# Optimization experiments

Hardware: AMD Instinct MI355X
Metric: run time of the kernel (lower is better)

The kernel has to match this reference:

```python
import jax, jax.numpy as jnp
import numpy as np

BN_EPS = 1e-5


def setup_inputs() -> dict:
    key = jax.random.key(0)
    ks = jax.random.split(key, 6)
    N_IN, N_OUT, K3, P, C_IN, C_OUT = 100000, 200000, 27, 80000, 64, 64
    features = jax.random.normal(ks[0], (N_IN, C_IN), dtype=jnp.float32)
    weight = jax.random.normal(ks[1], (K3, C_IN, C_OUT), dtype=jnp.float32) * 0.05
    bias = jnp.zeros((C_OUT,), dtype=jnp.float32)
    gamma = jnp.ones((C_OUT,), dtype=jnp.float32)
    beta = jnp.zeros((C_OUT,), dtype=jnp.float32)
    pairs_in = jax.random.randint(ks[2], (K3, P), 0, N_IN, dtype=jnp.int32)
    pairs_out = jax.random.randint(ks[3], (K3, P), 0, N_OUT, dtype=jnp.int32)
    return {
        "features": features, "weight": weight, "bias": bias,
        "gamma": gamma, "beta": beta,
        "pairs_in": pairs_in, "pairs_out": pairs_out, "n_out": N_OUT,
    }


def reference(features, weight, bias, gamma, beta, pairs_in, pairs_out, n_out):
    # --- SparseInverseConv3d: gather -> per-offset GEMM -> scatter-add ---
    C_out = weight.shape[2]
    gathered = features[pairs_in]                      # [K3, P, C_in]
    prod = jnp.einsum('kpc,kcd->kpd', gathered, weight)  # [K3, P, C_out]
    out = jnp.zeros((n_out, C_out), dtype=features.dtype)
    out = out.at[pairs_out.reshape(-1)].add(prod.reshape(-1, C_out))
    out = out + bias                                   # [N_out, C_out]
    # --- BatchNorm1d (training mode: batch stats, biased var) ---
    mean = jnp.mean(out, axis=0)
    var = jnp.var(out, axis=0)
    y = (out - mean) * jax.lax.rsqrt(var + BN_EPS) * gamma + beta
    # --- ReLU ---
    return jnp.maximum(y, 0.0)
```

## Files before the change

kernel.cpp:

```cpp
#include <hip/hip_runtime.h>
#include <hip/hip_fp16.h>


#define C_DIM 64
#define LDS_STRIDE 72
#define ROW_STRIDE 68

typedef __bf16 bf16_t;
typedef bf16_t bf16x4 __attribute__((ext_vector_type(4)));
typedef bf16_t bf16x8 __attribute__((ext_vector_type(8)));
typedef float floatx4 __attribute__((ext_vector_type(4)));

__global__ __launch_bounds__(256)
void k_fprep(const float* __restrict__ f, bf16_t* __restrict__ fb, int total4)
{
    int i = blockIdx.x * 256 + threadIdx.x;
    if (i < total4) {
        float4 v = ((const float4*)f)[i];
        bf16x4 o;
        o[0] = (bf16_t)v.x; o[1] = (bf16_t)v.y;
        o[2] = (bf16_t)v.z; o[3] = (bf16_t)v.w;
        ((bf16x4*)fb)[i] = o;
    }
}

__global__ __launch_bounds__(256)
void k1_fp16(const float* __restrict__ features,
             const bf16_t* __restrict__ fbf16,
             const float* __restrict__ weight,
             const int* __restrict__ pairs_in,
             const int* __restrict__ pairs_out,
             __half* __restrict__ acc,
             int P, int rows_per_block, int use_bf16)
{
    __shared__ bf16_t Wt[C_DIM * LDS_STRIDE];
    __shared__ float  scratch[4][16 * ROW_STRIDE];

    const int k   = blockIdx.y;
    const int tid = threadIdx.x;

    const float* Wk = weight + (size_t)k * C_DIM * C_DIM;
    for (int i = tid; i < C_DIM * C_DIM; i += 256) {
        int c = i >> 6, d = i & 63;
        Wt[d * LDS_STRIDE + c] = (bf16_t)Wk[i];
    }
    __syncthreads();

    const int wave = tid >> 6;
    const int lane = tid & 63;
    const int quad = lane >> 4;
    const int col  = lane & 15;
    const int sub  = lane >> 5;
    const int c2   = lane & 31;
    float* ls = &scratch[wave][0];

    bf16x8 bfrag[2][4];
    #pragma unroll
    for (int ks = 0; ks < 2; ++ks)
        #pragma unroll
        for (int nt = 0; nt < 4; ++nt)
            bfrag[ks][nt] =
                *(const bf16x8*)&Wt[(col + 16 * nt) * LDS_STRIDE + quad * 8 + 32 * ks];

    const int* __restrict__ pin  = pairs_in  + (size_t)k * P;
    const int* __restrict__ pout = pairs_out + (size_t)k * P;

    const int p0   = blockIdx.x * rows_per_block;
    const int pend = min(p0 + rows_per_block, P);

    for (int base = p0 + wave * 16; base < pend; base += 64) {
        int prow    = base + col;
        int clamped = (prow < pend) ? prow : (pend - 1);
        int in_idx  = pin[clamped];
        int out_idx = pout[clamped];

        bf16x8 a0, a1;
        if (use_bf16) {
            const bf16_t* src = fbf16 + (size_t)in_idx * C_DIM + quad * 8;
            a0 = *(const bf16x8*)(src);
            a1 = *(const bf16x8*)(src + 32);
        } else {
            const float* src = features + (size_t)in_idx * C_DIM + quad * 8;
            float4 f0 = *(const float4*)(src);
            float4 f1 = *(const float4*)(src + 4);
            float4 f2 = *(const float4*)(src + 32);
            float4 f3 = *(const float4*)(src + 36);
            a0[0] = (bf16_t)f0.x; a0[1] = (bf16_t)f0.y; a0[2] = (bf16_t)f0.z; a0[3] = (bf16_t)f0.w;
            a0[4] = (bf16_t)f1.x; a0[5] = (bf16_t)f1.y; a0[6] = (bf16_t)f1.z; a0[7] = (bf16_t)f1.w;
            a1[0] = (bf16_t)f2.x; a1[1] = (bf16_t)f2.y; a1[2] = (bf16_t)f2.z; a1[3] = (bf16_t)f2.w;
            a1[4] = (bf16_t)f3.x; a1[5] = (bf16_t)f3.y; a1[6] = (bf16_t)f3.z; a1[7] = (bf16_t)f3.w;
        }

        floatx4 acc0 = {0.f, 0.f, 0.f, 0.f};
        floatx4 acc1 = {0.f, 0.f, 0.f, 0.f};
        floatx4 acc2 = {0.f, 0.f, 0.f, 0.f};
        floatx4 acc3 = {0.f, 0.f, 0.f, 0.f};

        acc0 = __builtin_amdgcn_mfma_f32_16x16x32_bf16(a0, bfrag[0][0], acc0, 0, 0, 0);
        acc0 = __builtin_amdgcn_mfma_f32_16x16x32_bf16(a1, bfrag[1][0], acc0, 0, 0, 0);
        acc1 = __builtin_amdgcn_mfma_f32_16x16x32_bf16(a0, bfrag[0][1], acc1, 0, 0, 0);
        acc1 = __builtin_amdgcn_mfma_f32_16x16x32_bf16(a1, bfrag[1][1], acc1, 0, 0, 0);
        acc2 = __builtin_amdgcn_mfma_f32_16x16x32_bf16(a0, bfrag[0][2], acc2, 0, 0, 0);
        acc2 = __builtin_amdgcn_mfma_f32_16x16x32_bf16(a1, bfrag[1][2], acc2, 0, 0, 0);
        acc3 = __builtin_amdgcn_mfma_f32_16x16x32_bf16(a0, bfrag[0][3], acc3, 0, 0, 0);
        acc3 = __builtin_amdgcn_mfma_f32_16x16x32_bf16(a1, bfrag[1][3], acc3, 0, 0, 0);

        #pragma unroll
        for (int r = 0; r < 4; ++r) {
            int m = quad * 4 + r;
            ls[m * ROW_STRIDE + col +  0] = acc0[r];
            ls[m * ROW_STRIDE + col + 16] = acc1[r];
            ls[m * ROW_STRIDE + col + 32] = acc2[r];
            ls[m * ROW_STRIDE + col + 48] = acc3[r];
        }
        asm volatile("s_waitcnt lgkmcnt(0)" ::: "memory");

        #pragma unroll
        for (int m2 = 0; m2 < 8; ++m2) {
            int m = m2 * 2 + sub;
            float2 v = *(const float2*)&ls[m * ROW_STRIDE + 2 * c2];
            __half2 h = __floats2half2_rn(v.x, v.y);
            int g = __shfl(out_idx, m);
            if (base + m < pend)
                unsafeAtomicAdd((__half2*)(acc + (size_t)g * C_DIM + 2 * c2), h);
        }
    }
}

__global__ __launch_bounds__(256)
void k2_stats_h(const __half* __restrict__ acc, float* __restrict__ sums,
                int n_rows)
{
    const int tid = threadIdx.x;
    const int c2  = tid & 31;
    const int sub = tid >> 5;

    float s0 = 0.f, s1 = 0.f, q0 = 0.f, q1 = 0.f;
    for (int r = blockIdx.x * 8 + sub; r < n_rows; r += gridDim.x * 8) {
        __half2 v = *(const __half2*)&acc[(size_t)r * C_DIM + 2 * c2];
        float x = __half2float(v.x), y = __half2float(v.y);
        s0 += x; q0 += x * x;
        s1 += y; q1 += y * y;
    }

    __shared__ float red[128];
    if (tid < 128) red[tid] = 0.f;
    __syncthreads();
    atomicAdd(&red[2 * c2], s0);
    atomicAdd(&red[2 * c2 + 1], s1);
    atomicAdd(&red[64 + 2 * c2], q0);
    atomicAdd(&red[64 + 2 * c2 + 1], q1);
    __syncthreads();
    if (tid < 128) atomicAdd(&sums[tid], red[tid]);
}

__global__ __launch_bounds__(256)
void k3_bn_relu_h(const __half* __restrict__ acc, float* __restrict__ out,
                  const float* __restrict__ sums,
                  const float* __restrict__ gamma, const float* __restrict__ beta,
                  int n_rows)
{
    int tid = blockIdx.x * 256 + threadIdx.x;
    int c2  = tid & 31;
    float inv_n = 1.0f / (float)n_rows;

    float sc[2], sh[2];
    #pragma unroll
    for (int j = 0; j < 2; ++j) {
        int ch    = 2 * c2 + j;
        float m   = sums[ch] * inv_n;
        float var = sums[64 + ch] * inv_n - m * m;
        float inv = rsqrtf(var + 1e-5f);
        float g   = gamma[ch] * inv;
        sc[j] = g;
        sh[j] = beta[ch] - m * g;
    }

    size_t total = (size_t)n_rows * (C_DIM / 2);
    for (size_t i = tid; i < total; i += (size_t)gridDim.x * 256) {
        __half2 v = ((const __half2*)acc)[i];
        float2 o;
        o.x = fmaxf(__half2float(v.x) * sc[0] + sh[0], 0.f);
        o.y = fmaxf(__half2float(v.y) * sc[1] + sh[1], 0.f);
        ((float2*)out)[i] = o;
    }
}

__global__ __launch_bounds__(256)
void k1_scatter_gemm(const float* __restrict__ features,
                     const float* __restrict__ weight,
                     const int* __restrict__ pairs_in,
                     const int* __restrict__ pairs_out,
                     float* __restrict__ out,
                     int P, int rows_per_block)
{
    __shared__ bf16_t Wt[C_DIM * LDS_STRIDE];
    const int k   = blockIdx.y;
    const int tid = threadIdx.x;
    const float* Wk = weight + (size_t)k * C_DIM * C_DIM;
    for (int i = tid; i < C_DIM * C_DIM; i += 256) {
        int c = i >> 6, d = i & 63;
        Wt[d * LDS_STRIDE + c] = (bf16_t)Wk[i];
    }
    __syncthreads();
    const int wave = tid >> 6, lane = tid & 63, quad = lane >> 4, col = lane & 15;
    bf16x8 bfrag[2][4];
    #pragma unroll
    for (int ks = 0; ks < 2; ++ks)
        #pragma unroll
        for (int nt = 0; nt < 4; ++nt)
            bfrag[ks][nt] =
                *(const bf16x8*)&Wt[(col + 16 * nt) * LDS_STRIDE + quad * 8 + 32 * ks];
    const int* __restrict__ pin  = pairs_in  + (size_t)k * P;
    const int* __restrict__ pout = pairs_out + (size_t)k * P;
    const int p0   = blockIdx.x * rows_per_block;
    const int pend = min(p0 + rows_per_block, P);
    for (int base = p0 + wave * 16; base < pend; base += 64) {
        int prow    = base + col;
        int clamped = (prow < pend) ? prow : (pend - 1);
        int in_idx  = pin[clamped];
        int out_idx = pout[clamped];
        const float* src = features + (size_t)in_idx * C_DIM + quad * 8;
        float4 f0 = *(const float4*)(src);
        float4 f1 = *(const float4*)(src + 4);
        float4 f2 = *(const float4*)(src + 32);
        float4 f3 = *(const float4*)(src + 36);
        bf16x8 a0, a1;
        a0[0] = (bf16_t)f0.x; a0[1] = (bf16_t)f0.y; a0[2] = (bf16_t)f0.z; a0[3] = (bf16_t)f0.w;
        a0[4] = (bf16_t)f1.x; a0[5] = (bf16_t)f1.y; a0[6] = (bf16_t)f1.z; a0[7] = (bf16_t)f1.w;
        a1[0] = (bf16_t)f2.x; a1[1] = (bf16_t)f2.y; a1[2] = (bf16_t)f2.z; a1[3] = (bf16_t)f2.w;
        a1[4] = (bf16_t)f3.x; a1[5] = (bf16_t)f3.y; a1[6] = (bf16_t)f3.z; a1[7] = (bf16_t)f3.w;
        floatx4 acc0 = {0.f,0.f,0.f,0.f}, acc1 = {0.f,0.f,0.f,0.f};
        floatx4 acc2 = {0.f,0.f,0.f,0.f}, acc3 = {0.f,0.f,0.f,0.f};
        acc0 = __builtin_amdgcn_mfma_f32_16x16x32_bf16(a0, bfrag[0][0], acc0, 0, 0, 0);
        acc0 = __builtin_amdgcn_mfma_f32_16x16x32_bf16(a1, bfrag[1][0], acc0, 0, 0, 0);
        acc1 = __builtin_amdgcn_mfma_f32_16x16x32_bf16(a0, bfrag[0][1], acc1, 0, 0, 0);
        acc1 = __builtin_amdgcn_mfma_f32_16x16x32_bf16(a1, bfrag[1][1], acc1, 0, 0, 0);
        acc2 = __builtin_amdgcn_mfma_f32_16x16x32_bf16(a0, bfrag[0][2], acc2, 0, 0, 0);
        acc2 = __builtin_amdgcn_mfma_f32_16x16x32_bf16(a1, bfrag[1][2], acc2, 0, 0, 0);
        acc3 = __builtin_amdgcn_mfma_f32_16x16x32_bf16(a0, bfrag[0][3], acc3, 0, 0, 0);
        acc3 = __builtin_amdgcn_mfma_f32_16x16x32_bf16(a1, bfrag[1][3], acc3, 0, 0, 0);
        #pragma unroll
        for (int r = 0; r < 4; ++r) {
            int m = quad * 4 + r;
            int g = __shfl(out_idx, m);
            if (base + m < pend) {
                float* dst = out + (size_t)g * C_DIM + col;
                unsafeAtomicAdd(dst +  0, acc0[r]);
                unsafeAtomicAdd(dst + 16, acc1[r]);
                unsafeAtomicAdd(dst + 32, acc2[r]);
                unsafeAtomicAdd(dst + 48, acc3[r]);
            }
        }
    }
}

__global__ __launch_bounds__(256)
void k2_stats(const float* __restrict__ acc, float* __restrict__ sums, int n_rows)
{
    int tid = threadIdx.x;
    int ch  = tid & 63;
    int sub = tid >> 6;
    float s = 0.f, s2 = 0.f;
    for (int r = blockIdx.x * 4 + sub; r < n_rows; r += gridDim.x * 4) {
        float v = acc[(size_t)r * C_DIM + ch];
        s  += v;
        s2 += v * v;
    }
    __shared__ float red[256];
    red[tid] = s;
    __syncthreads();
    if (tid < 64) {
        float t = red[tid] + red[tid + 64] + red[tid + 128] + red[tid + 192];
        atomicAdd(&sums[ch], t);
    }
    __syncthreads();
    red[tid] = s2;
    __syncthreads();
    if (tid < 64) {
        float t = red[tid] + red[tid + 64] + red[tid + 128] + red[tid + 192];
        atomicAdd(&sums[64 + ch], t);
    }
}

__global__ __launch_bounds__(256)
void k3_bn_relu(float* __restrict__ out, const float* __restrict__ sums,
                const float* __restrict__ gamma, const float* __restrict__ beta,
                int n_rows)
{
    int tid = blockIdx.x * 256 + threadIdx.x;
    int ch0 = (tid * 4) & 63;
    float inv_n = 1.0f / (float)n_rows;
    float sc[4], sh[4];
    #pragma unroll
    for (int j = 0; j < 4; ++j) {
        int ch    = ch0 + j;
        float m   = sums[ch] * inv_n;
        float var = sums[64 + ch] * inv_n - m * m;
        float inv = rsqrtf(var + 1e-5f);
        float g   = gamma[ch] * inv;
        sc[j] = g;
        sh[j] = beta[ch] - m * g;
    }
    size_t total = (size_t)n_rows * C_DIM / 4;
    for (size_t i = tid; i < total; i += (size_t)gridDim.x * 256) {
        float4 v = ((const float4*)out)[i];
        v.x = fmaxf(v.x * sc[0] + sh[0], 0.f);
        v.y = fmaxf(v.y * sc[1] + sh[1], 0.f);
        v.z = fmaxf(v.z * sc[2] + sh[2], 0.f);
        v.w = fmaxf(v.w * sc[3] + sh[3], 0.f);
        ((float4*)out)[i] = v;
    }
}

extern "C" void kernel_launch(void* const* d_in, const int* in_sizes, int n_in,
                              void* d_out, int out_size, void* d_ws, size_t ws_size,
                              hipStream_t stream)
{
    const float* features  = (const float*)d_in[0];
    const float* weight    = (const float*)d_in[1];
    const float* gamma     = (const float*)d_in[3];
    const float* beta      = (const float*)d_in[4];
    const int*   pairs_in  = (const int*)d_in[5];
    const int*   pairs_out = (const int*)d_in[6];

    const int n_out     = out_size / C_DIM;
    const int n_in_rows = in_sizes[0] / C_DIM;
    const int K3        = in_sizes[1] / (C_DIM * C_DIM);
    const int P         = in_sizes[5] / K3;

    float* out = (float*)d_out;

    size_t acc_bytes = (size_t)n_out * C_DIM * 2;
    size_t off_acc   = 512;
    size_t off_fb    = (off_acc + acc_bytes + 255) & ~(size_t)255;
    size_t fb_bytes  = (size_t)n_in_rows * C_DIM * 2;
    size_t need_b    = off_acc + acc_bytes;
    size_t need_a    = off_fb + fb_bytes;

    float*  sums  = (float*)d_ws;
    __half* acc   = (__half*)((char*)d_ws + off_acc);
    bf16_t* fbf16 = (bf16_t*)((char*)d_ws + off_fb);

    const int rows_per_block = 512;
    dim3 g1((P + rows_per_block - 1) / rows_per_block, K3);

    if (ws_size >= need_b) {
        const int use_bf16 = (ws_size >= need_a) ? 1 : 0;

        hipMemsetAsync(sums, 0, 512, stream);
        hipMemsetAsync(acc, 0, acc_bytes, stream);
        if (use_bf16)
            k_fprep<<<(n_in_rows * 16 + 255) / 256, 256, 0, stream>>>(
                features, fbf16, n_in_rows * 16);

        k1_fp16<<<g1, 256, 0, stream>>>(features, fbf16, weight, pairs_in,
                                        pairs_out, acc, P, rows_per_block,
                                        use_bf16);

        k2_stats_h<<<dim3(1024), 256, 0, stream>>>(acc, sums, n_out);
        k3_bn_relu_h<<<dim3(1024), 256, 0, stream>>>(acc, out, sums, gamma,
                                                     beta, n_out);
    } else {
        hipMemsetAsync(d_out, 0, (size_t)out_size * sizeof(float), stream);
        hipMemsetAsync(d_ws, 0, 512, stream);

        k1_scatter_gemm<<<g1, 256, 0, stream>>>(features, weight, pairs_in,
                                                pairs_out, out, P, rows_per_block);
        k2_stats<<<dim3(1024), 256, 0, stream>>>(out, sums, n_out);
        k3_bn_relu<<<dim3(1024), 256, 0, stream>>>(out, sums, gamma, beta, n_out);
    }
}
```

Before: 367.1 us.

## Compute transposed MFMA tile so each lane scatters its own row directly

The operands of the MFMA are swapped so the output comes out transposed: each lane holds four consecutive channels of one output row. It then issues eight half2 atomics straight to global memory, dropping the LDS scratch round-trip, the wait and the index shuffles. The stats and BN/ReLU kernels are widened to 16-byte loads covering 8 channels per thread, and their grid sizes are reduced. The two memsets are merged into one. The atomics are now scattered as 4-byte pieces per lane rather than as contiguous 128-byte row segments per wave, which may change how well atomic traffic coalesces.

```diff
diff --git a/kernel.cpp b/kernel.cpp
--- a/kernel.cpp
+++ b/kernel.cpp
@@ -4,7 +4,6 @@
 
 #define C_DIM 64
 #define LDS_STRIDE 72
-#define ROW_STRIDE 68
 
 typedef __bf16 bf16_t;
 typedef bf16_t bf16x4 __attribute__((ext_vector_type(4)));
@@ -25,16 +24,15 @@
 }
 
 __global__ __launch_bounds__(256)
-void k1_fp16(const float* __restrict__ features,
-             const bf16_t* __restrict__ fbf16,
-             const float* __restrict__ weight,
-             const int* __restrict__ pairs_in,
-             const int* __restrict__ pairs_out,
-             __half* __restrict__ acc,
-             int P, int rows_per_block, int use_bf16)
+void k1_ct(const float* __restrict__ features,
+           const bf16_t* __restrict__ fbf16,
+           const float* __restrict__ weight,
+           const int* __restrict__ pairs_in,
+           const int* __restrict__ pairs_out,
+           __half* __restrict__ acc,
+           int P, int rows_per_block, int use_bf16)
 {
     __shared__ bf16_t Wt[C_DIM * LDS_STRIDE];
-    __shared__ float  scratch[4][16 * ROW_STRIDE];
 
     const int k   = blockIdx.y;
     const int tid = threadIdx.x;
@@ -50,16 +48,13 @@
     const int lane = tid & 63;
     const int quad = lane >> 4;
     const int col  = lane & 15;
-    const int sub  = lane >> 5;
-    const int c2   = lane & 31;
-    float* ls = &scratch[wave][0];
-
-    bf16x8 bfrag[2][4];
+
+    bf16x8 wfrag[2][4];
     #pragma unroll
     for (int ks = 0; ks < 2; ++ks)
         #pragma unroll
         for (int nt = 0; nt < 4; ++nt)
-            bfrag[ks][nt] =
+            wfrag[ks][nt] =
                 *(const bf16x8*)&Wt[(col + 16 * nt) * LDS_STRIDE + quad * 8 + 32 * ks];
 
     const int* __restrict__ pin  = pairs_in  + (size_t)k * P;
@@ -91,38 +86,31 @@
             a1[4] = (bf16_t)f3.x; a1[5] = (bf16_t)f3.y; a1[6] = (bf16_t)f3.z; a1[7] = (bf16_t)f3.w;
         }
 
-        floatx4 acc0 = {0.f, 0.f, 0.f, 0.f};
-        floatx4 acc1 = {0.f, 0.f, 0.f, 0.f};
-        floatx4 acc2 = {0.f, 0.f, 0.f, 0.f};
-        floatx4 acc3 = {0.f, 0.f, 0.f, 0.f};
-
-        acc0 = __builtin_amdgcn_mfma_f32_16x16x32_bf16(a0, bfrag[0][0], acc0, 0, 0, 0);
-        acc0 = __builtin_amdgcn_mfma_f32_16x16x32_bf16(a1, bfrag[1][0], acc0, 0, 0, 0);
-        acc1 = __builtin_amdgcn_mfma_f32_16x16x32_bf16(a0, bfrag[0][1], acc1, 0, 0, 0);
-        acc1 = __builtin_amdgcn_mfma_f32_16x16x32_bf16(a1, bfrag[1][1], acc1, 0, 0, 0);
-        acc2 = __builtin_amdgcn_mfma_f32_16x16x32_bf16(a0, bfrag[0][2], acc2, 0, 0, 0);
-        acc2 = __builtin_amdgcn_mfma_f32_16x16x32_bf16(a1, bfrag[1][2], acc2, 0, 0, 0);
-        acc3 = __builtin_amdgcn_mfma_f32_16x16x32_bf16(a0, bfrag[0][3], acc3, 0, 0, 0);
-        acc3 = __builtin_amdgcn_mfma_f32_16x16x32_bf16(a1, bfrag[1][3], acc3, 0, 0, 0);
-
-        #pragma unroll
-        for (int r = 0; r < 4; ++r) {
-            int m = quad * 4 + r;
-            ls[m * ROW_STRIDE + col +  0] = acc0[r];
-            ls[m * ROW_STRIDE + col + 16] = acc1[r];
-            ls[m * ROW_STRIDE + col + 32] = acc2[r];
-            ls[m * ROW_STRIDE + col + 48] = acc3[r];
-        }
-        asm volatile("s_waitcnt lgkmcnt(0)" ::: "memory");
-
-        #pragma unroll
-        for (int m2 = 0; m2 < 8; ++m2) {
-            int m = m2 * 2 + sub;
-            float2 v = *(const float2*)&ls[m * ROW_STRIDE + 2 * c2];
-            __half2 h = __floats2half2_rn(v.x, v.y);
-            int g = __shfl(out_idx, m);
-            if (base + m < pend)
-                unsafeAtomicAdd((__half2*)(acc + (size_t)g * C_DIM + 2 * c2), h);
+        floatx4 ac0 = {0.f, 0.f, 0.f, 0.f};
+        floatx4 ac1 = {0.f, 0.f, 0.f, 0.f};
+        floatx4 ac2 = {0.f, 0.f, 0.f, 0.f};
+        floatx4 ac3 = {0.f, 0.f, 0.f, 0.f};
+
+        ac0 = __builtin_amdgcn_mfma_f32_16x16x32_bf16(wfrag[0][0], a0, ac0, 0, 0, 0);
+        ac0 = __builtin_amdgcn_mfma_f32_16x16x32_bf16(wfrag[1][0], a1, ac0, 0, 0, 0);
+        ac1 = __builtin_amdgcn_mfma_f32_16x16x32_bf16(wfrag[0][1], a0, ac1, 0, 0, 0);
+        ac1 = __builtin_amdgcn_mfma_f32_16x16x32_bf16(wfrag[1][1], a1, ac1, 0, 0, 0);
+        ac2 = __builtin_amdgcn_mfma_f32_16x16x32_bf16(wfrag[0][2], a0, ac2, 0, 0, 0);
+        ac2 = __builtin_amdgcn_mfma_f32_16x16x32_bf16(wfrag[1][2], a1, ac2, 0, 0, 0);
+        ac3 = __builtin_amdgcn_mfma_f32_16x16x32_bf16(wfrag[0][3], a0, ac3, 0, 0, 0);
+        ac3 = __builtin_amdgcn_mfma_f32_16x16x32_bf16(wfrag[1][3], a1, ac3, 0, 0, 0);
+
+        if (prow < pend) {
+            __half* dst = acc + (size_t)out_idx * C_DIM + 4 * quad;
+            __half2 h;
+            h = __floats2half2_rn(ac0[0], ac0[1]); unsafeAtomicAdd((__half2*)(dst +  0), h);
+            h = __floats2half2_rn(ac0[2], ac0[3]); unsafeAtomicAdd((__half2*)(dst +  2), h);
+            h = __floats2half2_rn(ac1[0], ac1[1]); unsafeAtomicAdd((__half2*)(dst + 16), h);
+            h = __floats2half2_rn(ac1[2], ac1[3]); unsafeAtomicAdd((__half2*)(dst + 18), h);
+            h = __floats2half2_rn(ac2[0], ac2[1]); unsafeAtomicAdd((__half2*)(dst + 32), h);
+            h = __floats2half2_rn(ac2[2], ac2[3]); unsafeAtomicAdd((__half2*)(dst + 34), h);
+            h = __floats2half2_rn(ac3[0], ac3[1]); unsafeAtomicAdd((__half2*)(dst + 48), h);
+            h = __floats2half2_rn(ac3[2], ac3[3]); unsafeAtomicAdd((__half2*)(dst + 50), h);
         }
     }
 }
@@ -132,24 +120,29 @@
                 int n_rows)
 {
     const int tid = threadIdx.x;
-    const int c2  = tid & 31;
-    const int sub = tid >> 5;
-
-    float s0 = 0.f, s1 = 0.f, q0 = 0.f, q1 = 0.f;
-    for (int r = blockIdx.x * 8 + sub; r < n_rows; r += gridDim.x * 8) {
-        __half2 v = *(const __half2*)&acc[(size_t)r * C_DIM + 2 * c2];
-        float x = __half2float(v.x), y = __half2float(v.y);
-        s0 += x; q0 += x * x;
-        s1 += y; q1 += y * y;
+    const int c8  = tid & 7;
+    const int sub = tid >> 3;
+
+    float s[8] = {0,0,0,0,0,0,0,0}, q[8] = {0,0,0,0,0,0,0,0};
+    for (int r = blockIdx.x * 32 + sub; r < n_rows; r += gridDim.x * 32) {
+        float4 v = *(const float4*)&acc[(size_t)r * C_DIM + c8 * 8];
+        const __half2* h = (const __half2*)&v;
+        #pragma unroll
+        for (int j = 0; j < 4; ++j) {
+            float x = __half2float(h[j].x), y = __half2float(h[j].y);
+            s[2*j]   += x; q[2*j]   += x * x;
+            s[2*j+1] += y; q[2*j+1] += y * y;
+        }
     }
 
     __shared__ float red[128];
     if (tid < 128) red[tid] = 0.f;
     __syncthreads();
-    atomicAdd(&red[2 * c2], s0);
-    atomicAdd(&red[2 * c2 + 1], s1);
-    atomicAdd(&red[64 + 2 * c2], q0);
-    atomicAdd(&red[64 + 2 * c2 + 1], q1);
+    #pragma unroll
+    for (int j = 0; j < 8; ++j) {
+        atomicAdd(&red[c8 * 8 + j], s[j]);
+        atomicAdd(&red[64 + c8 * 8 + j], q[j]);
+    }
     __syncthreads();
     if (tid < 128) atomicAdd(&sums[tid], red[tid]);
 }
@@ -161,13 +154,13 @@
                   int n_rows)
 {
     int tid = blockIdx.x * 256 + threadIdx.x;
-    int c2  = tid & 31;
+    int c8  = tid & 7;
     float inv_n = 1.0f / (float)n_rows;
 
-    float sc[2], sh[2];
-    #pragma unroll
-    for (int j = 0; j < 2; ++j) {
-        int ch    = 2 * c2 + j;
+    float sc[8], sh[8];
+    #pragma unroll
+    for (int j = 0; j < 8; ++j) {
+        int ch    = c8 * 8 + j;
         float m   = sums[ch] * inv_n;
         float var = sums[64 + ch] * inv_n - m * m;
         float inv = rsqrtf(var + 1e-5f);
@@ -176,13 +169,21 @@
         sh[j] = beta[ch] - m * g;
     }
 
-    size_t total = (size_t)n_rows * (C_DIM / 2);
+    size_t total = (size_t)n_rows * 8;
     for (size_t i = tid; i < total; i += (size_t)gridDim.x * 256) {
-        __half2 v = ((const __half2*)acc)[i];
-        float2 o;
-        o.x = fmaxf(__half2float(v.x) * sc[0] + sh[0], 0.f);
-        o.y = fmaxf(__half2float(v.y) * sc[1] + sh[1], 0.f);
-        ((float2*)out)[i] = o;
+        float4 v = ((const float4*)acc)[i];
+        const __half2* h = (const __half2*)&v;
+        float4 o0, o1;
+        o0.x = fmaxf(__half2float(h[0].x) * sc[0] + sh[0], 0.f);
+        o0.y = fmaxf(__half2float(h[0].y) * sc[1] + sh[1], 0.f);
+        o0.z = fmaxf(__half2float(h[1].x) * sc[2] + sh[2], 0.f);
+        o0.w = fmaxf(__half2float(h[1].y) * sc[3] + sh[3], 0.f);
+        o1.x = fmaxf(__half2float(h[2].x) * sc[4] + sh[4], 0.f);
+        o1.y = fmaxf(__half2float(h[2].y) * sc[5] + sh[5], 0.f);
+        o1.z = fmaxf(__half2float(h[3].x) * sc[6] + sh[6], 0.f);
+        o1.w = fmaxf(__half2float(h[3].y) * sc[7] + sh[7], 0.f);
+        ((float4*)out)[2 * i]     = o0;
+        ((float4*)out)[2 * i + 1] = o1;
     }
 }
 
@@ -348,19 +349,18 @@
     if (ws_size >= need_b) {
         const int use_bf16 = (ws_size >= need_a) ? 1 : 0;
 
-        hipMemsetAsync(sums, 0, 512, stream);
-        hipMemsetAsync(acc, 0, acc_bytes, stream);
+        hipMemsetAsync(d_ws, 0, off_acc + acc_bytes, stream);
         if (use_bf16)
             k_fprep<<<(n_in_rows * 16 + 255) / 256, 256, 0, stream>>>(
                 features, fbf16, n_in_rows * 16);
 
-        k1_fp16<<<g1, 256, 0, stream>>>(features, fbf16, weight, pairs_in,
-                                        pairs_out, acc, P, rows_per_block,
-                                        use_bf16);
-
-        k2_stats_h<<<dim3(1024), 256, 0, stream>>>(acc, sums, n_out);
-        k3_bn_relu_h<<<dim3(1024), 256, 0, stream>>>(acc, out, sums, gamma,
-                                                     beta, n_out);
+        k1_ct<<<g1, 256, 0, stream>>>(features, fbf16, weight, pairs_in,
+                                      pairs_out, acc, P, rows_per_block,
+                                      use_bf16);
+
+        k2_stats_h<<<dim3(256), 256, 0, stream>>>(acc, sums, n_out);
+        k3_bn_relu_h<<<dim3(512), 256, 0, stream>>>(acc, out, sums, gamma,
+                                                    beta, n_out);
     } else {
         hipMemsetAsync(d_out, 0, (size_t)out_size * sizeof(float), stream);
         hipMemsetAsync(d_ws, 0, 512, stream);
```

Result: slower. 1.011 ms (+175.3%).
